# Performance work log

Measured on AMD Instinct MI355X. Metric: run time of the kernel, lower is better.

Reference implementation:

```python
import jax, jax.numpy as jnp
import numpy as np

PATCH = 3      # patch_size = (3, 3)
STRIDE = 1     # filter_patch_stride == compare_stride == 1
EPS = 1e-12    # F.normalize eps


def extract_patches(x, ph, pw, stride):
    """x: (B, C, H, W) -> (B, nH*nW, C, ph, pw), valid patches."""
    B, C, H, W = x.shape
    oh = (H - ph) // stride + 1
    ow = (W - pw) // stride + 1
    rows = (jnp.arange(oh) * stride)[:, None] + jnp.arange(ph)[None, :]  # (oh, ph)
    cols = (jnp.arange(ow) * stride)[:, None] + jnp.arange(pw)[None, :]  # (ow, pw)
    # gather -> (B, C, oh, ph, ow, pw)
    p = x[:, :, rows[:, :, None, None], cols[None, None, :, :]]
    return p.transpose(0, 2, 4, 1, 3, 5).reshape(B, oh * ow, C, ph, pw)


def l2norm(x, axis):
    # matches F.normalize(p=2): x / max(||x||, eps)
    return x / jnp.maximum(jnp.linalg.norm(x, axis=axis, keepdims=True), EPS)


def setup_inputs() -> dict:
    key = jax.random.key(0)
    k1, k2 = jax.random.split(key)
    pred_style = jax.random.normal(k1, (4, 256, 64, 64), dtype=jnp.float32)
    target_style = jax.random.normal(k2, (4, 256, 64, 64), dtype=jnp.float32)
    return {"pred_style": pred_style, "target_style": target_style}


def reference(pred_style, target_style):
    # patches of the raw (unnormalized) features
    tp = extract_patches(target_style, PATCH, PATCH, STRIDE)   # (B, nP, C, ph, pw)
    pp = extract_patches(pred_style, PATCH, PATCH, STRIDE)     # (B, nP, C, ph, pw)

    # best_match: normalize content feature over channels, style patches over channel dim (dim=2)
    x1n = l2norm(pred_style, axis=1)
    tpn = l2norm(tp, axis=2)
    x1p = extract_patches(x1n, PATCH, PATCH, STRIDE)           # (B, nP, C, ph, pw)

    # conv-as-cosine-correlation == batched patch dot products, then argmax over style patches
    scores = jnp.einsum('bqcij,bpcij->bqp', x1p, tpn)          # (B, nP, nP)
    match = jnp.argmax(scores, axis=2)                         # (B, nP)

    # gather best-matching target patches (indices detached in original via .data)
    new_t = jnp.take_along_axis(tp, match[:, :, None, None, None], axis=1)
    return jnp.mean((pp - new_t) ** 2)
```

## Files before the change

kernel.cpp:

```cpp
#include <hip/hip_runtime.h>
#include <hip/hip_bf16.h>

#define NB 4
#define CH 256
#define HH 64
#define WW 64
#define NPIX 4096
#define OH 62
#define NPATCH 3844
#define KDIM 256
#define EPSN 1e-12f
#define VROW 68
#define SEG 16

typedef __attribute__((ext_vector_type(8))) short short8;
typedef __attribute__((ext_vector_type(4))) float f32x4;

__device__ __forceinline__ float bf16_to_f32(unsigned short u) {
    return __uint_as_float((unsigned)u << 16);
}
__device__ __forceinline__ unsigned short f32_to_bf16(float f) {
    __hip_bfloat16 h = __float2bfloat16(f);
    return *(unsigned short*)&h;
}

__global__ __launch_bounds__(256) void k_prep(const float* __restrict__ pred,
                                              const float* __restrict__ tgt,
                                              __hip_bfloat16* __restrict__ Xn,
                                              __hip_bfloat16* __restrict__ Tn,
                                              float* __restrict__ ssP, float* __restrict__ invP,
                                              float* __restrict__ ssT, float* __restrict__ invT,
                                              unsigned long long* __restrict__ keys,
                                              float* __restrict__ out) {
    const int bz = blockIdx.y;
    const int b = bz >> 1, which = bz & 1;
    const float* src = (which ? tgt : pred) + (size_t)b * CH * NPIX;
    unsigned short* dst = (unsigned short*)((which ? Tn : Xn) + (size_t)b * NPIX * CH);
    float* ss_g  = (which ? ssT  : ssP)  + b * NPIX;
    float* inv_g = (which ? invT : invP) + b * NPIX;
    const int pix0 = blockIdx.x * 64;
    const int t = threadIdx.x, lane = t & 63, wv = t >> 6;

    int gid = (bz * 64 + blockIdx.x) * 256 + t;
    if (gid < NB * NPATCH) keys[gid] = 0ull;
    if (gid == 0) out[0] = 0.f;

    __shared__ unsigned short stage[CH][65];
    __shared__ float partial[4][64];
    __shared__ float inv_s[64];

    float ssacc = 0.f;
#pragma unroll 8
    for (int cc = 0; cc < 64; ++cc) {
        int c = wv * 64 + cc;
        float v = src[(size_t)c * NPIX + pix0 + lane];
        ssacc += v * v;
        stage[c][lane] = f32_to_bf16(v);
    }
    partial[wv][lane] = ssacc;
    __syncthreads();
    if (t < 64) {
        float ss = partial[0][t] + partial[1][t] + partial[2][t] + partial[3][t];
        float inv = 1.f / fmaxf(sqrtf(ss), EPSN);
        ss_g[pix0 + t] = ss;
        inv_g[pix0 + t] = inv;
        inv_s[t] = inv;
    }
    __syncthreads();
    for (int p = wv; p < 64; p += 4) {
        float iv = inv_s[p];
#pragma unroll
        for (int cb = 0; cb < 4; ++cb) {
            int c = cb * 64 + lane;
            float v = bf16_to_f32(stage[c][p]) * iv;
            dst[(size_t)(pix0 + p) * CH + c] = f32_to_bf16(v);
        }
    }
}

__device__ __forceinline__ void gload_lds16(const void* g, void* l) {
    __builtin_amdgcn_global_load_lds(
        (const __attribute__((address_space(1))) void*)g,
        (__attribute__((address_space(3))) void*)l, 16, 0, 0);
}

__global__ __launch_bounds__(512) void k_gemm(const __hip_bfloat16* __restrict__ A,
                                              const __hip_bfloat16* __restrict__ Bm,
                                              unsigned short* __restrict__ Dout) {
    __shared__ short As[2][8192];
    __shared__ short Bs[2][8192];
    const int z = blockIdx.z;
    const int t = threadIdx.x;
    const int lane = t & 63, wv = t >> 6;
    const int wm = wv >> 1, wn = wv & 1;
    const int row0 = blockIdx.y * 128, col0 = blockIdx.x * 128;
    const short* Ag = (const short*)A + (size_t)z * NPIX * CH;
    const short* Bg = (const short*)Bm + (size_t)z * NPIX * CH;
    unsigned short* D = Dout + (size_t)z * NPIX * NPIX;

    const int srow = t >> 3;
    const int kce  = ((t & 7) ^ (srow & 7)) * 8;

    f32x4 acc[2][4] = {};

#define STAGE_K(buf, k0)                                                                  \
    do {                                                                                  \
        gload_lds16(Ag + (size_t)(row0 + srow) * KDIM + (k0) + kce,      &As[buf][wv * 512]);        \
        gload_lds16(Ag + (size_t)(row0 + 64 + srow) * KDIM + (k0) + kce, &As[buf][4096 + wv * 512]); \
        gload_lds16(Bg + (size_t)(col0 + srow) * KDIM + (k0) + kce,      &Bs[buf][wv * 512]);        \
        gload_lds16(Bg + (size_t)(col0 + 64 + srow) * KDIM + (k0) + kce, &Bs[buf][4096 + wv * 512]); \
    } while (0)

    STAGE_K(0, 0);

    const int rsel = lane & 15, kq = lane >> 4;
    const int rx = rsel & 7;
#pragma unroll
    for (int it = 0; it < 4; ++it) {
        __syncthreads();
        const int buf = it & 1;
        if (it < 3) STAGE_K(buf ^ 1, (it + 1) * 64);
#pragma unroll
        for (int s = 0; s < 2; ++s) {
            const int pk = (((s << 2) + kq) ^ rx) * 8;
            short8 a[2], bfr[4];
#pragma unroll
            for (int mi = 0; mi < 2; ++mi)
                a[mi] = *(const short8*)&As[buf][(wm * 32 + mi * 16 + rsel) * 64 + pk];
#pragma unroll
            for (int ni = 0; ni < 4; ++ni)
                bfr[ni] = *(const short8*)&Bs[buf][(wn * 64 + ni * 16 + rsel) * 64 + pk];
#pragma unroll
            for (int mi = 0; mi < 2; ++mi)
#pragma unroll
                for (int ni = 0; ni < 4; ++ni)
                    acc[mi][ni] = __builtin_amdgcn_mfma_f32_16x16x32_bf16(a[mi], bfr[ni], acc[mi][ni], 0, 0, 0);
        }
    }
#undef STAGE_K
    const int rbase = (lane >> 4) * 4, cbase = lane & 15;
#pragma unroll
    for (int mi = 0; mi < 2; ++mi) {
#pragma unroll
        for (int ni = 0; ni < 4; ++ni) {
            int r0 = row0 + wm * 32 + mi * 16 + rbase;
            int c  = col0 + wn * 64 + ni * 16 + cbase;
#pragma unroll
            for (int r = 0; r < 4; ++r)
                D[(size_t)(r0 + r) * NPIX + c] = f32_to_bf16(acc[mi][ni][r]);
        }
    }
}

__device__ __forceinline__ void load_tile16(const unsigned short* __restrict__ D,
                                            int row, int col, float* f) {
    const unsigned short* rp = D + (size_t)row * NPIX + col;
    uint4 u0 = *(const uint4*)rp;
    uint4 u1 = *(const uint4*)(rp + 8);
    const unsigned* w0 = (const unsigned*)&u0;
    const unsigned* w1 = (const unsigned*)&u1;
#pragma unroll
    for (int w = 0; w < 4; ++w) {
        f[2 * w]         = bf16_to_f32((unsigned short)w0[w]);
        f[2 * w + 1]     = bf16_to_f32((unsigned short)(w0[w] >> 16));
        f[8 + 2 * w]     = bf16_to_f32((unsigned short)w1[w]);
        f[8 + 2 * w + 1] = bf16_to_f32((unsigned short)(w1[w] >> 16));
    }
}

__global__ __launch_bounds__(256) void k_score(const unsigned short* __restrict__ Dbase,
                                               unsigned long long* __restrict__ keys) {
    const int z = blockIdx.y;
    const unsigned short* D = Dbase + (size_t)z * NPIX * NPIX;
    const int t = threadIdx.x;

    const int bx = blockIdx.x;
    int d, s0;
    if (bx < 108)      { int q = bx >> 2;  d = q - 13;  s0 = (bx & 3) * SEG; }
    else if (bx < 204) { int r = bx - 108; int q = r / 3; int s = r - q * 3;
                         d = (q < 16) ? (14 + q) : -(q - 2);  s0 = s * SEG; }
    else if (bx < 268) { int r = bx - 204; int q = r >> 1;
                         d = (q < 16) ? (30 + q) : -(q + 14);  s0 = (r & 1) * SEG; }
    else               { int r = bx - 268;
                         d = (r < 16) ? (46 + r) : -(r + 30);  s0 = 0; }
    const int adg = d < 0 ? -d : d;
    const int len = 62 - adg;
    const int steps = min(SEG, len - s0);
    const int qr0 = (d > 0 ? d : 0) + s0;
    const int pr0 = qr0 - d;

    __shared__ __align__(16) float V[64 * VROW];

    const int a = t >> 2, b0 = (t & 3) * 16;
    const int g = t >> 6, qc = t & 63;
    const int qcr = qc < OH ? qc : (OH - 1);
    const int pc0 = g * 16;
    const int kmax = (g == 3) ? 14 : 16;

    float A[16], B[16], C[16];
    load_tile16(D, (qr0 + 0) * 64 + a, (pr0 + 0) * 64 + b0, A);
    load_tile16(D, (qr0 + 1) * 64 + a, (pr0 + 1) * 64 + b0, B);

    for (int k = 0; k < steps; ++k) {
        load_tile16(D, (qr0 + k + 2) * 64 + a, (pr0 + k + 2) * 64 + b0, C);
        float v[16];
#pragma unroll
        for (int e = 0; e < 16; ++e) v[e] = A[e] + B[e] + C[e];
        if (k) __syncthreads();
#pragma unroll
        for (int e = 0; e < 16; e += 4)
            *(f32x4*)&V[a * VROW + b0 + e] = *(const f32x4*)&v[e];
        __syncthreads();

        float r0[16], r1[20], r2[20];
#pragma unroll
        for (int e = 0; e < 16; e += 4)
            *(f32x4*)&r0[e] = *(const f32x4*)&V[qcr * VROW + pc0 + e];
#pragma unroll
        for (int e = 0; e < 20; e += 4)
            *(f32x4*)&r1[e] = *(const f32x4*)&V[(qcr + 1) * VROW + pc0 + e];
#pragma unroll
        for (int e = 0; e < 20; e += 4)
            *(f32x4*)&r2[e] = *(const f32x4*)&V[(qcr + 2) * VROW + pc0 + e];
        float best = -1e30f; int bpc = 0;
#pragma unroll
        for (int kk = 0; kk < 16; ++kk) {
            float s = r0[kk] + r1[kk + 1] + r2[kk + 2];
            if (kk < kmax && s > best) { best = s; bpc = pc0 + kk; }
        }
        if (qc < OH) {
            unsigned u = __float_as_uint(best);
            u = (best >= 0.f) ? (u | 0x80000000u) : ~u;
            unsigned long long key = ((unsigned long long)u << 12)
                                   | (unsigned)((63 - (pr0 + k)) << 6)
                                   | (unsigned)(63 - bpc);
            atomicMax(&keys[(size_t)z * NPATCH + (qr0 + k) * OH + qc], key);
        }
#pragma unroll
        for (int e = 0; e < 16; ++e) { A[e] = B[e]; B[e] = C[e]; }
    }
}

__global__ void k_loss(const unsigned short* __restrict__ Dbase,
                       const unsigned long long* __restrict__ keys,
                       const float* __restrict__ ssPb, const float* __restrict__ invPb,
                       const float* __restrict__ ssTb, const float* __restrict__ invTb,
                       float* __restrict__ out) {
    const int z = blockIdx.y;
    const unsigned short* D = Dbase + (size_t)z * NPIX * NPIX;
    const float* ssP  = ssPb  + z * NPIX;
    const float* invP = invPb + z * NPIX;
    const float* ssT  = ssTb  + z * NPIX;
    const float* invT = invTb + z * NPIX;
    int q = blockIdx.x * 256 + threadIdx.x;
    float acc = 0.f;
    if (q < NPATCH) {
        int qr = q / OH, qc = q - qr * OH;
        int qpix = qr * WW + qc;
        unsigned long long key = keys[(size_t)z * NPATCH + q];
        int mpr = 63 - (int)((key >> 6) & 63);
        int mpc = 63 - (int)(key & 63);
        int mpix = mpr * WW + mpc;
#pragma unroll
        for (int i = 0; i < 3; ++i)
#pragma unroll
            for (int j = 0; j < 3; ++j) {
                int off = i * WW + j;
                int y = qpix + off, x = mpix + off;
                float Dv = bf16_to_f32(D[(size_t)y * NPIX + x]);
                float nP = ssP[y] * invP[y];
                float nT = ssT[x] * invT[x];
                acc += ssP[y] + ssT[x] - 2.f * Dv * nP * nT;
            }
    }
#pragma unroll
    for (int s = 32; s > 0; s >>= 1) acc += __shfl_down(acc, s, 64);
    if ((threadIdx.x & 63) == 0)
        atomicAdd(out, acc * (1.f / 35426304.f));
}

extern "C" void kernel_launch(void* const* d_in, const int* in_sizes, int n_in,
                              void* d_out, int out_size, void* d_ws, size_t ws_size,
                              hipStream_t stream) {
    const float* pred = (const float*)d_in[0];
    const float* tgt  = (const float*)d_in[1];
    char* ws = (char*)d_ws;
    unsigned short*     Dws  = (unsigned short*)(ws);
    __hip_bfloat16*     Xn   = (__hip_bfloat16*)(ws + 134217728);
    __hip_bfloat16*     Tn   = (__hip_bfloat16*)(ws + 142606336);
    float*              ssP  = (float*)(ws + 150994944);
    float*              invP = (float*)(ws + 151060480);
    float*              ssT  = (float*)(ws + 151126016);
    float*              invT = (float*)(ws + 151191552);
    unsigned long long* keys = (unsigned long long*)(ws + 151257088);

    k_prep<<<dim3(64, 8), 256, 0, stream>>>(pred, tgt, Xn, Tn, ssP, invP, ssT, invT,
                                            keys, (float*)d_out);
    k_gemm<<<dim3(32, 32, 4), 512, 0, stream>>>(Xn, Tn, Dws);
    k_score<<<dim3(300, 4), 256, 0, stream>>>(Dws, keys);
    k_loss<<<dim3(16, 4), 256, 0, stream>>>(Dws, keys, ssP, invP, ssT, invT,
                                            (float*)d_out);
}
```

Before: 185.5 us.

## Vectorize prep loads and split score diagonals into finer segments

```diff
diff --git a/kernel.cpp b/kernel.cpp
--- a/kernel.cpp
+++ b/kernel.cpp
@@ -11,7 +11,8 @@
 #define KDIM 256
 #define EPSN 1e-12f
 #define VROW 68
-#define SEG 16
+#define SEG 8
+#define PST 68
 
 typedef __attribute__((ext_vector_type(8))) short short8;
 typedef __attribute__((ext_vector_type(4))) float f32x4;
@@ -45,22 +46,29 @@
     if (gid < NB * NPATCH) keys[gid] = 0ull;
     if (gid == 0) out[0] = 0.f;
 
-    __shared__ unsigned short stage[CH][65];
-    __shared__ float partial[4][64];
+    __shared__ unsigned short stage[CH][PST];
+    __shared__ float partial[16][68];
     __shared__ float inv_s[64];
 
-    float ssacc = 0.f;
-#pragma unroll 8
-    for (int cc = 0; cc < 64; ++cc) {
-        int c = wv * 64 + cc;
-        float v = src[(size_t)c * NPIX + pix0 + lane];
-        ssacc += v * v;
-        stage[c][lane] = f32_to_bf16(v);
-    }
-    partial[wv][lane] = ssacc;
+    const int cb = t >> 4, chk = t & 15;
+    float ss0 = 0.f, ss1 = 0.f, ss2 = 0.f, ss3 = 0.f;
+#pragma unroll
+    for (int r = 0; r < 16; ++r) {
+        int c = cb * 16 + r;
+        float4 v = *(const float4*)&src[(size_t)c * NPIX + pix0 + chk * 4];
+        ss0 += v.x * v.x; ss1 += v.y * v.y; ss2 += v.z * v.z; ss3 += v.w * v.w;
+        ushort4 sv;
+        sv.x = f32_to_bf16(v.x); sv.y = f32_to_bf16(v.y);
+        sv.z = f32_to_bf16(v.z); sv.w = f32_to_bf16(v.w);
+        *(ushort4*)&stage[c][chk * 4] = sv;
+    }
+    float4 pv; pv.x = ss0; pv.y = ss1; pv.z = ss2; pv.w = ss3;
+    *(float4*)&partial[cb][chk * 4] = pv;
     __syncthreads();
     if (t < 64) {
-        float ss = partial[0][t] + partial[1][t] + partial[2][t] + partial[3][t];
+        float ss = 0.f;
+#pragma unroll
+        for (int r = 0; r < 16; ++r) ss += partial[r][t];
         float inv = 1.f / fmaxf(sqrtf(ss), EPSN);
         ss_g[pix0 + t] = ss;
         inv_g[pix0 + t] = inv;
@@ -70,8 +78,8 @@
     for (int p = wv; p < 64; p += 4) {
         float iv = inv_s[p];
 #pragma unroll
-        for (int cb = 0; cb < 4; ++cb) {
-            int c = cb * 64 + lane;
+        for (int cc = 0; cc < 4; ++cc) {
+            int c = cc * 64 + lane;
             float v = bf16_to_f32(stage[c][p]) * iv;
             dst[(size_t)(pix0 + p) * CH + c] = f32_to_bf16(v);
         }
@@ -170,21 +178,15 @@
 
 __global__ __launch_bounds__(256) void k_score(const unsigned short* __restrict__ Dbase,
                                                unsigned long long* __restrict__ keys) {
-    const int z = blockIdx.y;
+    const int z = blockIdx.z;
     const unsigned short* D = Dbase + (size_t)z * NPIX * NPIX;
     const int t = threadIdx.x;
 
-    const int bx = blockIdx.x;
-    int d, s0;
-    if (bx < 108)      { int q = bx >> 2;  d = q - 13;  s0 = (bx & 3) * SEG; }
-    else if (bx < 204) { int r = bx - 108; int q = r / 3; int s = r - q * 3;
-                         d = (q < 16) ? (14 + q) : -(q - 2);  s0 = s * SEG; }
-    else if (bx < 268) { int r = bx - 204; int q = r >> 1;
-                         d = (q < 16) ? (30 + q) : -(q + 14);  s0 = (r & 1) * SEG; }
-    else               { int r = bx - 268;
-                         d = (r < 16) ? (46 + r) : -(r + 30);  s0 = 0; }
+    const int d = (int)blockIdx.x - 61;
     const int adg = d < 0 ? -d : d;
     const int len = 62 - adg;
+    const int s0 = blockIdx.y * SEG;
+    if (s0 >= len) return;
     const int steps = min(SEG, len - s0);
     const int qr0 = (d > 0 ? d : 0) + s0;
     const int pr0 = qr0 - d;
@@ -297,7 +299,7 @@
     k_prep<<<dim3(64, 8), 256, 0, stream>>>(pred, tgt, Xn, Tn, ssP, invP, ssT, invT,
                                             keys, (float*)d_out);
     k_gemm<<<dim3(32, 32, 4), 512, 0, stream>>>(Xn, Tn, Dws);
-    k_score<<<dim3(300, 4), 256, 0, stream>>>(Dws, keys);
+    k_score<<<dim3(123, 8, 4), 256, 0, stream>>>(Dws, keys);
     k_loss<<<dim3(16, 4), 256, 0, stream>>>(Dws, keys, ssP, invP, ssT, invT,
                                             (float*)d_out);
 }
```

Result: faster. 175.6 us (-5.3%).
